# Kernel tuning notes

Hardware: AMD Instinct MI355X
Metric: run time of the kernel (lower is better)

Reference implementation:

```python
import jax, jax.numpy as jnp
import numpy as np

N_BINS = 18


def setup_inputs() -> dict:
    key = jax.random.key(0)
    k1, k2 = jax.random.split(key)
    B, C, Fp, Fa, S, T = 2, 16, 30, 50, 20, 1024
    # phase in [-pi, pi], amplitude positive
    pha = jax.random.uniform(k1, (B, C, Fp, S, T), jnp.float32, -np.pi, np.pi)
    amp = jax.random.uniform(k2, (B, C, Fa, S, T), jnp.float32, 0.0, 1.0)
    pha_bin_cutoffs = jnp.linspace(-np.pi, np.pi, N_BINS + 1).astype(jnp.float32)
    return {"pha": pha, "amp": amp, "pha_bin_cutoffs": pha_bin_cutoffs}


def reference(pha, amp, pha_bin_cutoffs):
    eps = 1e-9
    n_bins = pha_bin_cutoffs.shape[0] - 1
    # torch.bucketize(right=False) == searchsorted side='left'; then -1 and clamp
    bins = jnp.clip(
        jnp.searchsorted(pha_bin_cutoffs, pha, side="left") - 1, 0, n_bins - 1
    )  # (b,c,p,s,t)
    masks = jax.nn.one_hot(bins, n_bins, dtype=amp.dtype)  # (b,c,p,s,t,k)
    # scatter-sum of amplitudes into phase bins, contracted over time
    amp_sums = jnp.einsum("bcpstk,bcast->bcpask", masks, amp)  # (b,c,p,a,s,k)
    counts = masks.sum(axis=4)  # (b,c,p,s,k)
    amp_means = amp_sums / (counts[:, :, :, None, :, :] + eps)  # (b,c,p,a,s,k)
    amp_probs = amp_means / (amp_means.sum(axis=-1, keepdims=True) + eps)
    ent = (amp_probs * jnp.log(amp_probs + eps)).sum(axis=-1)  # (b,c,p,a,s)
    MI = (jnp.log(jnp.float32(n_bins) + eps) + ent) / jnp.log(jnp.float32(n_bins))
    return MI.mean(axis=-1)  # (b,c,p,a)
```

## Files before the change

### kernel.cpp

```cpp
#include <hip/hip_runtime.h>
#include <math.h>

#define NBINS 18
#define NB 2
#define NC 16
#define FP 30
#define FA 50
#define NS 20
#define NT 1024
#define TS 128
#define NCH (NT / TS)
#define PGSZ 15
#define NTHR 384
#define BSTR 136
#define BINSTR 136
#define ACCW 52

#define BIN_OFF (2 * 64 * BSTR * 2)
#define CUT_OFF (BIN_OFF + PGSZ * BINSTR)
#define SMEM_B (CUT_OFF + 19 * 4)

typedef __attribute__((ext_vector_type(8))) short bf16x8;
typedef __attribute__((ext_vector_type(4))) float f32x4;

__device__ inline float u2f(unsigned int u) { return __builtin_bit_cast(float, u); }
__device__ inline unsigned short f2bf(float x) {
    unsigned int u = __builtin_bit_cast(unsigned int, x);
    unsigned int r = (u + 0x7FFFu + ((u >> 16) & 1u)) >> 16;
    return (unsigned short)r;
}

__device__ __forceinline__ int bin_of(float v, const float* cl) {
    int b0 = __float2int_rd(fmaf(v, 2.86478897565f, 9.0f));
    b0 = b0 < 0 ? 0 : (b0 > 17 ? 17 : b0);
    const float lo = cl[b0];
    const float hi = cl[b0 + 1];
    return b0 + (int)((b0 < 17) & (hi < v)) - (int)((b0 > 0) & !(lo < v));
}

template <bool DIRECT>
__global__ __launch_bounds__(NTHR) void mi_mfma(const float* __restrict__ pha,
                                                const float* __restrict__ amp,
                                                const float* __restrict__ cut,
                                                float* __restrict__ outp) {
    __shared__ __align__(16) char smem[SMEM_B];
    short* Bh = (short*)smem;
    float* accs = (float*)smem;
    float* cl = (float*)(smem + CUT_OFF);

    const int g   = blockIdx.x;
    const int pg  = (g >> 3) & 1;
    const int bcs = (g >> 4) * 8 + (g & 7);
    const int s   = bcs % NS;
    const int bc  = bcs / NS;
    const int p0  = pg * PGSZ;

    const int tid  = threadIdx.x;
    const int lane = tid & 63;
    const int w    = tid >> 6;
    const int l16  = lane & 15;
    const int quad = lane >> 4;

    if (tid < 19) cl[tid] = cut[tid];

    int pm[3]; unsigned kx[3];
    #pragma unroll
    for (int mt = 0; mt < 3; ++mt) {
        const int row = w * 48 + mt * 16 + l16;
        const int valid = row < PGSZ * NBINS;
        const int p = valid ? (row / NBINS) : (PGSZ - 1);
        const int kb = valid ? (row - p * NBINS) : 31;
        pm[mt] = p;
        kx[mt] = (unsigned)kb * 0x01010101u;
    }

    for (int t = tid; t < TS; t += NTHR) {
        Bh[FA * BSTR + t] = (short)0x3F80;
        Bh[64 * BSTR + FA * BSTR + t] = 0;
    }

    f32x4 acc[3][4];
    #pragma unroll
    for (int mt = 0; mt < 3; ++mt)
        #pragma unroll
        for (int nt = 0; nt < 4; ++nt) acc[mt][nt] = (f32x4){0.f, 0.f, 0.f, 0.f};

    const size_t phabase0 = ((size_t)(bc * FP + p0) * NS + s) * NT;
    const size_t ampbase0 = ((size_t)bc * FA * NS + s) * NT;

    float4 ph_pf[2];
    float4 am_pf[5];

    auto LOAD = [&](int ch) {
        const float* pb = pha + phabase0 + ch * TS;
        #pragma unroll
        for (int r = 0; r < 2; ++r) {
            const int i = tid + r * NTHR;
            if (i < PGSZ * (TS / 4)) {
                const int p = i >> 5, tq = i & 31;
                ph_pf[r] = *(const float4*)(pb + (size_t)p * (NS * NT) + tq * 4);
            }
        }
        const float* ab = amp + ampbase0 + ch * TS;
        #pragma unroll
        for (int r = 0; r < 5; ++r) {
            const int i = tid + r * NTHR;
            if (i < FA * (TS / 4)) {
                const int a_ = i >> 5, tq = i & 31;
                am_pf[r] = *(const float4*)(ab + (size_t)a_ * (NS * NT) + tq * 4);
            }
        }
    };

    LOAD(0);

    for (int ch = 0; ch < NCH; ++ch) {
        __syncthreads();
        #pragma unroll
        for (int r = 0; r < 2; ++r) {
            const int i = tid + r * NTHR;
            if (i < PGSZ * (TS / 4)) {
                const int p = i >> 5, tq = i & 31;
                const float4 v4 = ph_pf[r];
                const unsigned pk = (unsigned)bin_of(v4.x, cl)
                                  | ((unsigned)bin_of(v4.y, cl) << 8)
                                  | ((unsigned)bin_of(v4.z, cl) << 16)
                                  | ((unsigned)bin_of(v4.w, cl) << 24);
                *(unsigned*)(smem + BIN_OFF + p * BINSTR + tq * 4) = pk;
            }
        }
        #pragma unroll
        for (int r = 0; r < 5; ++r) {
            const int i = tid + r * NTHR;
            if (i < FA * (TS / 4)) {
                const int a_ = i >> 5, tq = i & 31;
                const float4 v4 = am_pf[r];
                const unsigned short h0 = f2bf(v4.x), h1 = f2bf(v4.y);
                const unsigned short h2 = f2bf(v4.z), h3 = f2bf(v4.w);
                const unsigned short q0 = f2bf(v4.x - u2f((unsigned)h0 << 16));
                const unsigned short q1 = f2bf(v4.y - u2f((unsigned)h1 << 16));
                const unsigned short q2 = f2bf(v4.z - u2f((unsigned)h2 << 16));
                const unsigned short q3 = f2bf(v4.w - u2f((unsigned)h3 << 16));
                short* dst = Bh + a_ * BSTR + tq * 4;
                uint2 hv; hv.x = (unsigned)h0 | ((unsigned)h1 << 16); hv.y = (unsigned)h2 | ((unsigned)h3 << 16);
                uint2 lv; lv.x = (unsigned)q0 | ((unsigned)q1 << 16); lv.y = (unsigned)q2 | ((unsigned)q3 << 16);
                *(uint2*)dst = hv;
                *(uint2*)(dst + 64 * BSTR) = lv;
            }
        }
        __syncthreads();
        if (ch + 1 < NCH) LOAD(ch + 1);
        #pragma unroll
        for (int ks = 0; ks < 4; ++ks) {
            bf16x8 af[3];
            #pragma unroll
            for (int mt = 0; mt < 3; ++mt) {
                const uint2 d = *(const uint2*)(smem + BIN_OFF + pm[mt] * BINSTR + ks * 32 + quad * 8);
                const unsigned x0 = d.x ^ kx[mt];
                const unsigned x1 = d.y ^ kx[mt];
                const unsigned f0 = ~(x0 + 0x7F7F7F7Fu) & 0x80808080u;
                const unsigned f1 = ~(x1 + 0x7F7F7F7Fu) & 0x80808080u;
                uint4 a4;
                a4.x = (f0 & 0x80u) * 0x7Fu + ((f0 >> 8) & 0x80u) * 0x7F0000u;
                a4.y = ((f0 >> 16) & 0x80u) * 0x7Fu + (f0 >> 24) * 0x7F0000u;
                a4.z = (f1 & 0x80u) * 0x7Fu + ((f1 >> 8) & 0x80u) * 0x7F0000u;
                a4.w = ((f1 >> 16) & 0x80u) * 0x7Fu + (f1 >> 24) * 0x7F0000u;
                af[mt] = __builtin_bit_cast(bf16x8, a4);
            }
            bf16x8 bh[4], bl[4];
            #pragma unroll
            for (int nt = 0; nt < 4; ++nt) {
                const short* bp = Bh + (nt * 16 + l16) * BSTR + ks * 32 + quad * 8;
                bh[nt] = *(const bf16x8*)bp;
                bl[nt] = *(const bf16x8*)(bp + 64 * BSTR);
            }
            #pragma unroll
            for (int mt = 0; mt < 3; ++mt)
                #pragma unroll
                for (int nt = 0; nt < 4; ++nt)
                    acc[mt][nt] = __builtin_amdgcn_mfma_f32_16x16x32_bf16(af[mt], bh[nt], acc[mt][nt], 0, 0, 0);
            #pragma unroll
            for (int mt = 0; mt < 3; ++mt)
                #pragma unroll
                for (int nt = 0; nt < 4; ++nt)
                    acc[mt][nt] = __builtin_amdgcn_mfma_f32_16x16x32_bf16(af[mt], bl[nt], acc[mt][nt], 0, 0, 0);
        }
    }
    __syncthreads();

    const float ln18 = 2.8903717578961645f;
    const float inv_ln18 = 0.34598234401512115f;
    #pragma unroll 1
    for (int ph = 0; ph < 3; ++ph) {
        const int rlo = ph * 90, rhi = rlo + 90;
        #pragma unroll
        for (int mt = 0; mt < 3; ++mt) {
            #pragma unroll
            for (int nt = 0; nt < 4; ++nt) {
                const int col = nt * 16 + l16;
                if (col <= FA) {
                    #pragma unroll
                    for (int r2 = 0; r2 < 4; ++r2) {
                        const int row = w * 48 + mt * 16 + quad * 4 + r2;
                        if (row >= rlo && row < rhi)
                            accs[(row - rlo) * ACCW + col] = acc[mt][nt][r2];
                    }
                }
            }
        }
        __syncthreads();
        if (tid < 5 * FA) {
            const int pidx = tid / FA;
            const int a = tid - pidx * FA;
            float means[NBINS];
            float tot = 0.f;
            #pragma unroll
            for (int k = 0; k < NBINS; ++k) {
                const float sum = accs[(pidx * NBINS + k) * ACCW + a];
                const float cnt = accs[(pidx * NBINS + k) * ACCW + FA];
                const float m = sum / (cnt + 1e-9f);
                means[k] = m;
                tot += m;
            }
            const float rden = 1.0f / (tot + 1e-9f);
            float ent = 0.f;
            #pragma unroll
            for (int k = 0; k < NBINS; ++k) {
                const float pr = means[k] * rden;
                ent += pr * logf(pr + 1e-9f);
            }
            const float mi = (ln18 + ent) * inv_ln18;
            const int p = ph * 5 + pidx;
            const int oi = (bc * FP + p0 + p) * FA + a;
            if (DIRECT) {
                atomicAdd(&outp[oi], mi * (1.0f / NS));
            } else {
                outp[(size_t)s * (NB * NC * FP * FA) + oi] = mi;
            }
        }
        __syncthreads();
    }
}

__global__ void mi_reduce(const float* __restrict__ partial, float* __restrict__ out) {
    const int i = blockIdx.x * 256 + threadIdx.x;
    const int n = NB * NC * FP * FA;
    if (i < n) {
        float acc = 0.f;
        #pragma unroll
        for (int j = 0; j < NS; ++j) acc += partial[(size_t)j * n + i];
        out[i] = acc * (1.0f / NS);
    }
}

extern "C" void kernel_launch(void* const* d_in, const int* in_sizes, int n_in,
                              void* d_out, int out_size, void* d_ws, size_t ws_size,
                              hipStream_t stream) {
    const float* pha = (const float*)d_in[0];
    const float* amp = (const float*)d_in[1];
    const float* cut = (const float*)d_in[2];
    float* out = (float*)d_out;

    const int nout = NB * NC * FP * FA;
    const size_t need = (size_t)nout * NS * sizeof(float);
    const dim3 grid(NB * NC * NS * 2);

    if (ws_size >= need) {
        float* partial = (float*)d_ws;
        mi_mfma<false><<<grid, NTHR, 0, stream>>>(pha, amp, cut, partial);
        mi_reduce<<<(nout + 255) / 256, 256, 0, stream>>>(partial, out);
    } else {
        hipMemsetAsync(d_out, 0, (size_t)nout * sizeof(float), stream);
        mi_mfma<true><<<grid, NTHR, 0, stream>>>(pha, amp, cut, out);
    }
}
```

Measured before the change: 342.9 us.

## Double-buffer LDS staging so MFMA on one chunk overlaps staging the next

Splits LDS into two buffers for bf16 amplitude planes and packed bin indices. Each iteration now issues the next chunk's global loads, runs the MFMAs on the previous buffer, then stages the current chunk into the other buffer, so one barrier per chunk is needed instead of two. The hand-written bf16 rounding is replaced with the __float2bfloat16 intrinsic. In exchange the kernel uses about twice the shared memory, which may reduce occupancy, and the prefetch registers stay live across the MFMA phase.

```diff
diff --git a/kernel.cpp b/kernel.cpp
--- a/kernel.cpp
+++ b/kernel.cpp
@@ -1,4 +1,5 @@
 #include <hip/hip_runtime.h>
+#include <hip/hip_bf16.h>
 #include <math.h>
 
 #define NBINS 18
@@ -16,18 +17,19 @@
 #define BINSTR 136
 #define ACCW 52
 
-#define BIN_OFF (2 * 64 * BSTR * 2)
-#define CUT_OFF (BIN_OFF + PGSZ * BINSTR)
+#define PLANESH (64 * BSTR)
+#define BPLANES_B (2 * PLANESH * 2)
+#define BINB 2048
+#define BUF_B (BPLANES_B + BINB)
+#define CUT_OFF (2 * BUF_B)
 #define SMEM_B (CUT_OFF + 19 * 4)
 
 typedef __attribute__((ext_vector_type(8))) short bf16x8;
 typedef __attribute__((ext_vector_type(4))) float f32x4;
 
 __device__ inline float u2f(unsigned int u) { return __builtin_bit_cast(float, u); }
-__device__ inline unsigned short f2bf(float x) {
-    unsigned int u = __builtin_bit_cast(unsigned int, x);
-    unsigned int r = (u + 0x7FFFu + ((u >> 16) & 1u)) >> 16;
-    return (unsigned short)r;
+__device__ inline unsigned short bfr(float x) {
+    return __builtin_bit_cast(unsigned short, __float2bfloat16(x));
 }
 
 __device__ __forceinline__ int bin_of(float v, const float* cl) {
@@ -44,7 +46,6 @@
                                                 const float* __restrict__ cut,
                                                 float* __restrict__ outp) {
     __shared__ __align__(16) char smem[SMEM_B];
-    short* Bh = (short*)smem;
     float* accs = (float*)smem;
     float* cl = (float*)(smem + CUT_OFF);
 
@@ -75,8 +76,12 @@
     }
 
     for (int t = tid; t < TS; t += NTHR) {
-        Bh[FA * BSTR + t] = (short)0x3F80;
-        Bh[64 * BSTR + FA * BSTR + t] = 0;
+        #pragma unroll
+        for (int b = 0; b < 2; ++b) {
+            short* Bb = (short*)(smem + b * BUF_B);
+            Bb[FA * BSTR + t] = (short)0x3F80;
+            Bb[PLANESH + FA * BSTR + t] = 0;
+        }
     }
 
     f32x4 acc[3][4];
@@ -112,10 +117,7 @@
         }
     };
 
-    LOAD(0);
-
-    for (int ch = 0; ch < NCH; ++ch) {
-        __syncthreads();
+    auto STAGE = [&](char* sb) {
         #pragma unroll
         for (int r = 0; r < 2; ++r) {
             const int i = tid + r * NTHR;
@@ -126,36 +128,39 @@
                                   | ((unsigned)bin_of(v4.y, cl) << 8)
                                   | ((unsigned)bin_of(v4.z, cl) << 16)
                                   | ((unsigned)bin_of(v4.w, cl) << 24);
-                *(unsigned*)(smem + BIN_OFF + p * BINSTR + tq * 4) = pk;
-            }
-        }
+                *(unsigned*)(sb + BPLANES_B + p * BINSTR + tq * 4) = pk;
+            }
+        }
+        short* Bb = (short*)sb;
         #pragma unroll
         for (int r = 0; r < 5; ++r) {
             const int i = tid + r * NTHR;
             if (i < FA * (TS / 4)) {
                 const int a_ = i >> 5, tq = i & 31;
                 const float4 v4 = am_pf[r];
-                const unsigned short h0 = f2bf(v4.x), h1 = f2bf(v4.y);
-                const unsigned short h2 = f2bf(v4.z), h3 = f2bf(v4.w);
-                const unsigned short q0 = f2bf(v4.x - u2f((unsigned)h0 << 16));
-                const unsigned short q1 = f2bf(v4.y - u2f((unsigned)h1 << 16));
-                const unsigned short q2 = f2bf(v4.z - u2f((unsigned)h2 << 16));
-                const unsigned short q3 = f2bf(v4.w - u2f((unsigned)h3 << 16));
-                short* dst = Bh + a_ * BSTR + tq * 4;
+                const unsigned short h0 = bfr(v4.x), h1 = bfr(v4.y);
+                const unsigned short h2 = bfr(v4.z), h3 = bfr(v4.w);
+                const unsigned short q0 = bfr(v4.x - u2f((unsigned)h0 << 16));
+                const unsigned short q1 = bfr(v4.y - u2f((unsigned)h1 << 16));
+                const unsigned short q2 = bfr(v4.z - u2f((unsigned)h2 << 16));
+                const unsigned short q3 = bfr(v4.w - u2f((unsigned)h3 << 16));
+                short* dst = Bb + a_ * BSTR + tq * 4;
                 uint2 hv; hv.x = (unsigned)h0 | ((unsigned)h1 << 16); hv.y = (unsigned)h2 | ((unsigned)h3 << 16);
                 uint2 lv; lv.x = (unsigned)q0 | ((unsigned)q1 << 16); lv.y = (unsigned)q2 | ((unsigned)q3 << 16);
                 *(uint2*)dst = hv;
-                *(uint2*)(dst + 64 * BSTR) = lv;
-            }
-        }
-        __syncthreads();
-        if (ch + 1 < NCH) LOAD(ch + 1);
+                *(uint2*)(dst + PLANESH) = lv;
+            }
+        }
+    };
+
+    auto MFMA_PH = [&](const char* mb) {
+        const short* Bb = (const short*)mb;
         #pragma unroll
         for (int ks = 0; ks < 4; ++ks) {
             bf16x8 af[3];
             #pragma unroll
             for (int mt = 0; mt < 3; ++mt) {
-                const uint2 d = *(const uint2*)(smem + BIN_OFF + pm[mt] * BINSTR + ks * 32 + quad * 8);
+                const uint2 d = *(const uint2*)(mb + BPLANES_B + pm[mt] * BINSTR + ks * 32 + quad * 8);
                 const unsigned x0 = d.x ^ kx[mt];
                 const unsigned x1 = d.y ^ kx[mt];
                 const unsigned f0 = ~(x0 + 0x7F7F7F7Fu) & 0x80808080u;
@@ -170,9 +175,9 @@
             bf16x8 bh[4], bl[4];
             #pragma unroll
             for (int nt = 0; nt < 4; ++nt) {
-                const short* bp = Bh + (nt * 16 + l16) * BSTR + ks * 32 + quad * 8;
+                const short* bp = Bb + (nt * 16 + l16) * BSTR + ks * 32 + quad * 8;
                 bh[nt] = *(const bf16x8*)bp;
-                bl[nt] = *(const bf16x8*)(bp + 64 * BSTR);
+                bl[nt] = *(const bf16x8*)(bp + PLANESH);
             }
             #pragma unroll
             for (int mt = 0; mt < 3; ++mt)
@@ -185,8 +190,21 @@
                 for (int nt = 0; nt < 4; ++nt)
                     acc[mt][nt] = __builtin_amdgcn_mfma_f32_16x16x32_bf16(af[mt], bl[nt], acc[mt][nt], 0, 0, 0);
         }
-    }
+    };
+
+    LOAD(0);
     __syncthreads();
+    STAGE(smem);
+    for (int ch = 1; ch < NCH; ++ch) {
+        char* sb = smem + (ch & 1) * BUF_B;
+        const char* mb = smem + ((ch & 1) ^ 1) * BUF_B;
+        __syncthreads();
+        LOAD(ch);
+        MFMA_PH(mb);
+        STAGE(sb);
+    }
+    __syncthreads();
+    MFMA_PH(smem + BUF_B);
 
     const float ln18 = 2.8903717578961645f;
     const float inv_ln18 = 0.34598234401512115f;
```

Result: slower. 412.7 us (+20.4%).

## Precompute bf16 amplitude splits and phase bins, stream them via LDS-direct loads

Applied to the files above, without the earlier changes.

A new pre-pass kernel converts amplitudes into swizzled bf16 hi/lo tiles and phases into packed byte bin indices, both stored in workspace. The MFMA kernel then double-buffers these tiles into shared memory with global_load_lds and no longer does per-block conversion or binning. The goal is to take conversion ALU work and register staging out of the main kernel and overlap loads with MFMA. The cost is an extra full read and write of the amplitude data and a larger workspace requirement. The fallback path also replaces the table-lookup binning with a count of cutoffs held in registers.

```diff
diff --git a/kernel.cpp b/kernel.cpp
--- a/kernel.cpp
+++ b/kernel.cpp
@@ -1,4 +1,5 @@
 #include <hip/hip_runtime.h>
+#include <hip/hip_bf16.h>
 #include <math.h>
 
 #define NBINS 18
@@ -12,13 +13,6 @@
 #define NCH (NT / TS)
 #define PGSZ 15
 #define NTHR 384
-#define BSTR 136
-#define BINSTR 136
-#define ACCW 52
-
-#define BIN_OFF (2 * 64 * BSTR * 2)
-#define CUT_OFF (BIN_OFF + PGSZ * BINSTR)
-#define SMEM_B (CUT_OFF + 19 * 4)
 
 typedef __attribute__((ext_vector_type(8))) short bf16x8;
 typedef __attribute__((ext_vector_type(4))) float f32x4;
@@ -28,6 +22,9 @@
     unsigned int u = __builtin_bit_cast(unsigned int, x);
     unsigned int r = (u + 0x7FFFu + ((u >> 16) & 1u)) >> 16;
     return (unsigned short)r;
+}
+__device__ inline unsigned short bfr(float x) {
+    return __builtin_bit_cast(unsigned short, __float2bfloat16(x));
 }
 
 __device__ __forceinline__ int bin_of(float v, const float* cl) {
@@ -38,15 +35,79 @@
     return b0 + (int)((b0 < 17) & (hi < v)) - (int)((b0 > 0) & !(lo < v));
 }
 
+__device__ __forceinline__ void gl_lds16(const void* g, void* l) {
+    __builtin_amdgcn_global_load_lds(
+        (const __attribute__((address_space(1))) unsigned int*)g,
+        (__attribute__((address_space(3))) unsigned int*)l, 16, 0, 0);
+}
+
+#define NAMP4 8192000
+#define NPHA4 4915200
+
+__global__ __launch_bounds__(256) void mi_convert(const float* __restrict__ pha,
+                                                  const float* __restrict__ amp,
+                                                  const float* __restrict__ cut,
+                                                  uint2* __restrict__ wsAmp,
+                                                  unsigned* __restrict__ wsBin) {
+    __shared__ float cl[19];
+    if (threadIdx.x < 19) cl[threadIdx.x] = cut[threadIdx.x];
+    __syncthreads();
+    const int stride = gridDim.x * 256;
+    for (int idx = blockIdx.x * 256 + threadIdx.x; idx < NAMP4 + NPHA4; idx += stride) {
+        if (idx < NAMP4) {
+            const float4 v4 = *((const float4*)amp + idx);
+            const int t  = (idx & 255) << 2;
+            const int r  = idx >> 8;
+            const int s  = r % 20;
+            const int q  = r / 20;
+            const int a  = q % 50;
+            const int bc = q / 50;
+            const int ch = t >> 7, tc = t & 127;
+            const unsigned short h0 = bfr(v4.x), h1 = bfr(v4.y);
+            const unsigned short h2 = bfr(v4.z), h3 = bfr(v4.w);
+            const unsigned short q0 = bfr(v4.x - u2f((unsigned)h0 << 16));
+            const unsigned short q1 = bfr(v4.y - u2f((unsigned)h1 << 16));
+            const unsigned short q2 = bfr(v4.z - u2f((unsigned)h2 << 16));
+            const unsigned short q3 = bfr(v4.w - u2f((unsigned)h3 << 16));
+            uint2 hv, lv;
+            hv.x = (unsigned)h0 | ((unsigned)h1 << 16); hv.y = (unsigned)h2 | ((unsigned)h3 << 16);
+            lv.x = (unsigned)q0 | ((unsigned)q1 << 16); lv.y = (unsigned)q2 | ((unsigned)q3 << 16);
+            const size_t tile_u2 = (size_t)((bc * 20 + s) * NCH + ch) * 3200;
+            const int c4 = tc >> 3, half = (tc >> 2) & 1;
+            wsAmp[tile_u2 + (size_t)(a * 32 + c4) * 2 + half] = hv;
+            wsAmp[tile_u2 + (size_t)(a * 32 + 16 + c4) * 2 + half] = lv;
+        } else {
+            const int j = idx - NAMP4;
+            const float4 v4 = *((const float4*)pha + j);
+            const int t  = (j & 255) << 2;
+            const int r  = j >> 8;
+            const int s  = r % 20;
+            const int q  = r / 20;
+            const int p  = q % 30;
+            const int bc = q / 30;
+            const int ch = t >> 7, tc = t & 127;
+            const unsigned pk = (unsigned)bin_of(v4.x, cl)
+                              | ((unsigned)bin_of(v4.y, cl) << 8)
+                              | ((unsigned)bin_of(v4.z, cl) << 16)
+                              | ((unsigned)bin_of(v4.w, cl) << 24);
+            wsBin[(size_t)(((bc * FP + p) * NS + s) * NCH + ch) * 32 + (tc >> 2)] = pk;
+        }
+    }
+}
+
+#define ROWB 512
+#define AMPB (64 * ROWB)
+#define BINB2 2048
+#define BUFB (AMPB + BINB2)
+#define SMEM3 (2 * BUFB)
+#define ACCW 52
+
 template <bool DIRECT>
-__global__ __launch_bounds__(NTHR) void mi_mfma(const float* __restrict__ pha,
-                                                const float* __restrict__ amp,
-                                                const float* __restrict__ cut,
-                                                float* __restrict__ outp) {
-    __shared__ __align__(16) char smem[SMEM_B];
-    short* Bh = (short*)smem;
+__global__ __launch_bounds__(NTHR) void mi_mfma_pre(const uint4* __restrict__ wsAmp,
+                                                    const unsigned* __restrict__ wsBin,
+                                                    float* __restrict__ outp) {
+    __shared__ __align__(16) char smem[SMEM3];
     float* accs = (float*)smem;
-    float* cl = (float*)(smem + CUT_OFF);
 
     const int g   = blockIdx.x;
     const int pg  = (g >> 3) & 1;
@@ -60,8 +121,7 @@
     const int w    = tid >> 6;
     const int l16  = lane & 15;
     const int quad = lane >> 4;
-
-    if (tid < 19) cl[tid] = cut[tid];
+    const int x7   = l16 & 7;
 
     int pm[3]; unsigned kx[3];
     #pragma unroll
@@ -75,6 +135,190 @@
     }
 
     for (int t = tid; t < TS; t += NTHR) {
+        #pragma unroll
+        for (int b = 0; b < 2; ++b) {
+            short* rowp = (short*)(smem + b * BUFB + 50 * ROWB);
+            rowp[t] = (short)0x3F80;
+            rowp[128 + t] = 0;
+        }
+    }
+
+    f32x4 acc[3][4];
+    #pragma unroll
+    for (int mt = 0; mt < 3; ++mt)
+        #pragma unroll
+        for (int nt = 0; nt < 4; ++nt) acc[mt][nt] = (f32x4){0.f, 0.f, 0.f, 0.f};
+
+    const uint4* ampT = wsAmp + (size_t)bcs * (NCH * 1600);
+    const int binRow0 = (bc * FP + p0) * NS + s;
+
+    auto ISSUE = [&](int ch, int bsel) {
+        char* buf = smem + bsel * BUFB;
+        const uint4* at = ampT + ch * 1600;
+        #pragma unroll
+        for (int k = 0; k < 5; ++k) {
+            const int slot = w + 6 * k;
+            if (slot < 25) {
+                const int a  = 2 * slot + (lane >> 5);
+                const int pl = (lane >> 4) & 1;
+                const int cs = (lane & 15) ^ (a & 7);
+                gl_lds16(at + a * 32 + pl * 16 + cs, buf + slot * 1024);
+            } else if (slot < 27) {
+                const int jb = slot - 25;
+                int p_l = 8 * jb + (lane >> 3);
+                if (p_l > 14) p_l = 14;
+                const int c = lane & 7;
+                gl_lds16(wsBin + ((size_t)(binRow0 + p_l * NS) * NCH + ch) * 32 + c * 4,
+                         buf + AMPB + jb * 1024);
+            }
+        }
+    };
+
+    auto MFMA_PH = [&](int bsel) {
+        const char* buf = smem + bsel * BUFB;
+        #pragma unroll
+        for (int ks = 0; ks < 4; ++ks) {
+            bf16x8 af[3];
+            #pragma unroll
+            for (int mt = 0; mt < 3; ++mt) {
+                const uint2 d = *(const uint2*)(buf + AMPB + pm[mt] * 128 + ks * 32 + quad * 8);
+                const unsigned x0 = d.x ^ kx[mt];
+                const unsigned x1 = d.y ^ kx[mt];
+                const unsigned f0 = ~(x0 + 0x7F7F7F7Fu) & 0x80808080u;
+                const unsigned f1 = ~(x1 + 0x7F7F7F7Fu) & 0x80808080u;
+                uint4 a4;
+                a4.x = (f0 & 0x80u) * 0x7Fu + ((f0 >> 8) & 0x80u) * 0x7F0000u;
+                a4.y = ((f0 >> 16) & 0x80u) * 0x7Fu + (f0 >> 24) * 0x7F0000u;
+                a4.z = (f1 & 0x80u) * 0x7Fu + ((f1 >> 8) & 0x80u) * 0x7F0000u;
+                a4.w = ((f1 >> 16) & 0x80u) * 0x7Fu + (f1 >> 24) * 0x7F0000u;
+                af[mt] = __builtin_bit_cast(bf16x8, a4);
+            }
+            const int cidx = (4 * ks + quad) ^ x7;
+            bf16x8 bh[4], bl[4];
+            #pragma unroll
+            for (int nt = 0; nt < 4; ++nt) {
+                const char* bp = buf + (nt * 16 + l16) * ROWB + cidx * 16;
+                bh[nt] = *(const bf16x8*)bp;
+                bl[nt] = *(const bf16x8*)(bp + 256);
+            }
+            #pragma unroll
+            for (int mt = 0; mt < 3; ++mt)
+                #pragma unroll
+                for (int nt = 0; nt < 4; ++nt)
+                    acc[mt][nt] = __builtin_amdgcn_mfma_f32_16x16x32_bf16(af[mt], bh[nt], acc[mt][nt], 0, 0, 0);
+            #pragma unroll
+            for (int mt = 0; mt < 3; ++mt)
+                #pragma unroll
+                for (int nt = 0; nt < 4; ++nt)
+                    acc[mt][nt] = __builtin_amdgcn_mfma_f32_16x16x32_bf16(af[mt], bl[nt], acc[mt][nt], 0, 0, 0);
+        }
+    };
+
+    ISSUE(0, 0);
+    for (int ch = 0; ch < NCH; ++ch) {
+        __syncthreads();
+        if (ch + 1 < NCH) ISSUE(ch + 1, (ch + 1) & 1);
+        MFMA_PH(ch & 1);
+    }
+    __syncthreads();
+
+    const float ln18 = 2.8903717578961645f;
+    const float inv_ln18 = 0.34598234401512115f;
+    #pragma unroll 1
+    for (int ph = 0; ph < 3; ++ph) {
+        const int rlo = ph * 90, rhi = rlo + 90;
+        #pragma unroll
+        for (int mt = 0; mt < 3; ++mt) {
+            #pragma unroll
+            for (int nt = 0; nt < 4; ++nt) {
+                const int col = nt * 16 + l16;
+                if (col <= FA) {
+                    #pragma unroll
+                    for (int r2 = 0; r2 < 4; ++r2) {
+                        const int row = w * 48 + mt * 16 + quad * 4 + r2;
+                        if (row >= rlo && row < rhi)
+                            accs[(row - rlo) * ACCW + col] = acc[mt][nt][r2];
+                    }
+                }
+            }
+        }
+        __syncthreads();
+        if (tid < 5 * FA) {
+            const int pidx = tid / FA;
+            const int a = tid - pidx * FA;
+            float means[NBINS];
+            float tot = 0.f;
+            #pragma unroll
+            for (int k = 0; k < NBINS; ++k) {
+                const float sum = accs[(pidx * NBINS + k) * ACCW + a];
+                const float cnt = accs[(pidx * NBINS + k) * ACCW + FA];
+                const float m = sum / (cnt + 1e-9f);
+                means[k] = m;
+                tot += m;
+            }
+            const float rden = 1.0f / (tot + 1e-9f);
+            float ent = 0.f;
+            #pragma unroll
+            for (int k = 0; k < NBINS; ++k) {
+                const float pr = means[k] * rden;
+                ent += pr * logf(pr + 1e-9f);
+            }
+            const float mi = (ln18 + ent) * inv_ln18;
+            const int p = ph * 5 + pidx;
+            const int oi = (bc * FP + p0 + p) * FA + a;
+            if (DIRECT) {
+                atomicAdd(&outp[oi], mi * (1.0f / NS));
+            } else {
+                outp[(size_t)s * (NB * NC * FP * FA) + oi] = mi;
+            }
+        }
+        __syncthreads();
+    }
+}
+
+#define BSTR 136
+#define BINSTR 136
+#define BIN_OFF (2 * 64 * BSTR * 2)
+#define SMEM_B (BIN_OFF + PGSZ * BINSTR)
+
+template <bool DIRECT>
+__global__ __launch_bounds__(NTHR) void mi_mfma(const float* __restrict__ pha,
+                                                const float* __restrict__ amp,
+                                                const float* __restrict__ cut,
+                                                float* __restrict__ outp) {
+    __shared__ __align__(16) char smem[SMEM_B];
+    short* Bh = (short*)smem;
+    float* accs = (float*)smem;
+
+    const int g   = blockIdx.x;
+    const int pg  = (g >> 3) & 1;
+    const int bcs = (g >> 4) * 8 + (g & 7);
+    const int s   = bcs % NS;
+    const int bc  = bcs / NS;
+    const int p0  = pg * PGSZ;
+
+    const int tid  = threadIdx.x;
+    const int lane = tid & 63;
+    const int w    = tid >> 6;
+    const int l16  = lane & 15;
+    const int quad = lane >> 4;
+
+    float cuts[NBINS];
+    #pragma unroll
+    for (int j = 1; j <= 17; ++j) cuts[j] = cut[j];
+
+    int pm[3]; unsigned kx[3];
+    #pragma unroll
+    for (int mt = 0; mt < 3; ++mt) {
+        const int row = w * 48 + mt * 16 + l16;
+        const int valid = row < PGSZ * NBINS;
+        const int p = valid ? (row / NBINS) : (PGSZ - 1);
+        const int kb = valid ? (row - p * NBINS) : 31;
+        pm[mt] = p;
+        kx[mt] = (unsigned)kb * 0x01010101u;
+    }
+
+    for (int t = tid; t < TS; t += NTHR) {
         Bh[FA * BSTR + t] = (short)0x3F80;
         Bh[64 * BSTR + FA * BSTR + t] = 0;
     }
@@ -122,10 +366,16 @@
             if (i < PGSZ * (TS / 4)) {
                 const int p = i >> 5, tq = i & 31;
                 const float4 v4 = ph_pf[r];
-                const unsigned pk = (unsigned)bin_of(v4.x, cl)
-                                  | ((unsigned)bin_of(v4.y, cl) << 8)
-                                  | ((unsigned)bin_of(v4.z, cl) << 16)
-                                  | ((unsigned)bin_of(v4.w, cl) << 24);
+                int b0 = 0, b1 = 0, b2 = 0, b3 = 0;
+                #pragma unroll
+                for (int j = 1; j <= 17; ++j) {
+                    b0 += (cuts[j] < v4.x) ? 1 : 0;
+                    b1 += (cuts[j] < v4.y) ? 1 : 0;
+                    b2 += (cuts[j] < v4.z) ? 1 : 0;
+                    b3 += (cuts[j] < v4.w) ? 1 : 0;
+                }
+                const unsigned pk = (unsigned)b0 | ((unsigned)b1 << 8)
+                                  | ((unsigned)b2 << 16) | ((unsigned)b3 << 24);
                 *(unsigned*)(smem + BIN_OFF + p * BINSTR + tq * 4) = pk;
             }
         }
@@ -262,10 +512,20 @@
     float* out = (float*)d_out;
 
     const int nout = NB * NC * FP * FA;
-    const size_t need = (size_t)nout * NS * sizeof(float);
+    const size_t needP = (size_t)nout * NS * sizeof(float);
+    const size_t WSAMP = (size_t)NAMP4 * 16;
+    const size_t WSBIN = (size_t)NPHA4 * 4;
+    const size_t need2 = needP + WSAMP + WSBIN;
     const dim3 grid(NB * NC * NS * 2);
 
-    if (ws_size >= need) {
+    if (ws_size >= need2) {
+        float* partial = (float*)d_ws;
+        uint2* wsAmp = (uint2*)((char*)d_ws + needP);
+        unsigned* wsBin = (unsigned*)((char*)d_ws + needP + WSAMP);
+        mi_convert<<<2048, 256, 0, stream>>>(pha, amp, cut, wsAmp, wsBin);
+        mi_mfma_pre<false><<<grid, NTHR, 0, stream>>>((const uint4*)wsAmp, wsBin, partial);
+        mi_reduce<<<(nout + 255) / 256, 256, 0, stream>>>(partial, out);
+    } else if (ws_size >= needP) {
         float* partial = (float*)d_ws;
         mi_mfma<false><<<grid, NTHR, 0, stream>>>(pha, amp, cut, partial);
         mi_reduce<<<(nout + 255) / 256, 256, 0, stream>>>(partial, out);
```

Result: slower. 420.3 us (+22.6%).
